# Performance work log

Hardware: AMD Instinct MI355X
Metric: run time of the kernel (lower is better)

Reference implementation:

```python
import jax, jax.numpy as jnp
import numpy as np

N_NODES = 100000
K_NBRS = 16
N_EDGES = N_NODES * K_NBRS


def setup_inputs() -> dict:
    key = jax.random.key(0)
    ks = jax.random.split(key, 20)
    x = jax.random.normal(ks[0], (N_NODES, 3), dtype=jnp.float32)
    # knn-like edge list: every node is the target of exactly K_NBRS edges
    dst = jnp.repeat(jnp.arange(N_NODES, dtype=jnp.int64), K_NBRS)
    src = jax.random.randint(ks[1], (N_EDGES,), 0, N_NODES, dtype=jnp.int64)
    edge_index = jnp.stack([src, dst], axis=0)  # [2, E], row0=source(j), row1=target(i)

    def lin_init(k, fan_in, fan_out):
        s = 1.0 / np.sqrt(fan_in)
        return jax.random.uniform(k, (fan_in, fan_out), jnp.float32, -s, s)

    inp = {"x": x, "edge_index": edge_index}
    inp["W1"], inp["b1"] = lin_init(ks[2], 6, 64), jnp.zeros((64,), jnp.float32)
    for i, kk in zip(range(2, 6), ks[3:7]):
        inp[f"W{i}"] = lin_init(kk, 128, 64)
        inp[f"b{i}"] = jnp.zeros((64,), jnp.float32)
    inp["Wa"], inp["ba"] = lin_init(ks[8], 128, 128), jnp.zeros((128,), jnp.float32)
    inp["Wb"], inp["bb"] = lin_init(ks[9], 128, 3), jnp.zeros((3,), jnp.float32)
    return inp


def edge_conv(x, src, dst, W, b):
    # PyG EdgeConv: message = nn(cat([x_i, x_j - x_i])), max-aggregate at target i
    xi = x[dst]                      # [E, C] center (target) features
    xj = x[src]                      # [E, C] neighbor (source) features
    msg = jnp.concatenate([xi, xj - xi], axis=-1)  # [E, 2C]
    msg = jax.nn.relu(msg @ W + b)                 # [E, 64] per-edge MLP
    return jax.ops.segment_max(msg, dst, num_segments=N_NODES)  # [N, 64]


def reference(x, edge_index, W1, b1, W2, b2, W3, b3, W4, b4, W5, b5, Wa, ba, Wb, bb):
    src, dst = edge_index[0], edge_index[1]
    h = edge_conv(x, src, dst, W1, b1)
    h = edge_conv(h, src, dst, W2, b2)
    h = edge_conv(h, src, dst, W3, b3)
    h = edge_conv(h, src, dst, W4, b4)
    h = edge_conv(h, src, dst, W5, b5)           # [N, 64]
    g = jnp.max(h, axis=0, keepdims=True)        # [1, 64] global max
    feat = jnp.concatenate([h, jnp.broadcast_to(g, h.shape)], axis=1)  # [N, 128]
    out = jax.nn.relu(feat @ Wa + ba) @ Wb + bb  # [N, 3]
    return x + out
```

## Files before the change

### kernel.cpp

```cpp
#include <hip/hip_runtime.h>
#include <math.h>

#define N_NODES 100000
#define K_NBRS 16
#define N_EDGES (N_NODES * K_NBRS)
#define TPB 256
#define NBLK 2048
#define NTILES (N_NODES / 16)

typedef __attribute__((ext_vector_type(8))) short short8;
typedef __attribute__((ext_vector_type(4))) float float4_;
typedef __attribute__((ext_vector_type(4))) int int4_;
typedef __attribute__((ext_vector_type(4))) unsigned short ushort4_;

__device__ __forceinline__ unsigned short f2bf(float f) {
  unsigned int u = __float_as_uint(f);
  u += 0x7fffu + ((u >> 16) & 1u);
  return (unsigned short)(u >> 16);
}
__device__ __forceinline__ float bf2f(unsigned short b) {
  return __uint_as_float(((unsigned int)b) << 16);
}

__global__ void k_pre(const int* __restrict__ ei, int* __restrict__ srcout,
                      const float* __restrict__ x, const float* __restrict__ W1,
                      const float* __restrict__ b1,
                      unsigned short* __restrict__ A, unsigned short* __restrict__ B) {
  const bool is64 = (ei[1] == 0) && (ei[3] == 0) && (ei[5] == 0) && (ei[7] == 0);
  const int tid = blockIdx.x * blockDim.x + threadIdx.x;
  const int stride = gridDim.x * blockDim.x;
  for (int e = tid; e < N_EDGES; e += stride)
    srcout[e] = is64 ? ei[2 * e] : ei[e];

  const int lane = threadIdx.x & 63;
  const int nwaves = stride >> 6;
  const int wid0 = tid >> 6;
  float w[6];
#pragma unroll
  for (int k = 0; k < 6; ++k) w[k] = W1[k * 64 + lane];
  const float bias = b1[lane];
  for (int i0 = wid0; i0 < N_NODES; i0 += nwaves) {
    const int i = __builtin_amdgcn_readfirstlane(i0);
    const float x0 = x[3 * i], x1 = x[3 * i + 1], x2 = x[3 * i + 2];
    const float b = fmaf(x0, w[3], fmaf(x1, w[4], x2 * w[5]));
    const float a = bias + fmaf(x0, w[0] - w[3],
                          fmaf(x1, w[1] - w[4], x2 * (w[2] - w[5])));
    A[(size_t)i * 64 + lane] = f2bf(a);
    B[(size_t)i * 64 + lane] = f2bf(b);
  }
}

__global__ __launch_bounds__(TPB, 4)
void k_fused(const int* __restrict__ src,
             const unsigned short* __restrict__ Ain,
             const unsigned short* __restrict__ Bin,
             const float* __restrict__ W, const float* __restrict__ bn,
             unsigned short* __restrict__ Aout, unsigned short* __restrict__ Bout) {
  __shared__ __align__(16) unsigned short lwhi[128 * 72];
  __shared__ __align__(16) unsigned short lwlo[128 * 72];
  __shared__ __align__(16) unsigned short lh[16 * 72];
  for (int idx = threadIdx.x; idx < 8192; idx += TPB) {
    const int k = idx >> 7, j = idx & 127;
    const float v = (j < 64) ? (W[k * 64 + j] - W[(64 + k) * 64 + j])
                             : W[(64 + k) * 64 + (j - 64)];
    const unsigned short hi = f2bf(v);
    lwhi[j * 72 + k] = hi;
    lwlo[j * 72 + k] = f2bf(v - bf2f(hi));
  }
  const int lane = threadIdx.x & 63;
  const int wav = threadIdx.x >> 6;
  const int q = lane >> 4;
  const int l15 = lane & 15;
  const int c4 = l15 * 4;
  float bv0 = 0.f, bv1 = 0.f;
  if (wav < 2) {
    bv0 = bn[(2 * wav) * 16 + l15];
    bv1 = bn[(2 * wav + 1) * 16 + l15];
  }
  __syncthreads();
  for (int t = blockIdx.x; t < NTILES; t += gridDim.x) {
    const int i0 = t * 16 + wav * 4;
    int4_ idx[4];
#pragma unroll
    for (int n = 0; n < 4; ++n)
      idx[n] = *(const int4_*)(src + (size_t)(i0 + n) * 16 + q * 4);
    ushort4_ gv[4][4];
#pragma unroll
    for (int n = 0; n < 4; ++n)
#pragma unroll
      for (int e = 0; e < 4; ++e)
        gv[n][e] = *(const ushort4_*)(Bin + (size_t)idx[n][e] * 64 + c4);
    const ushort4_ av = *(const ushort4_*)(Ain + (size_t)(i0 + q) * 64 + c4);
    float4_ m[4];
#pragma unroll
    for (int n = 0; n < 4; ++n) {
#pragma unroll
      for (int tt = 0; tt < 4; ++tt) {
        const float v0 = bf2f(gv[n][0][tt]), v1 = bf2f(gv[n][1][tt]);
        const float v2 = bf2f(gv[n][2][tt]), v3 = bf2f(gv[n][3][tt]);
        m[n][tt] = fmaxf(fmaxf(v0, v1), fmaxf(v2, v3));
      }
#pragma unroll
      for (int tt = 0; tt < 4; ++tt) {
        float v = m[n][tt];
        v = fmaxf(v, __shfl_xor(v, 16));
        v = fmaxf(v, __shfl_xor(v, 32));
        m[n][tt] = v;
      }
    }
    ushort4_ hb;
#pragma unroll
    for (int tt = 0; tt < 4; ++tt) {
      float v = m[0][tt];
      v = (q == 1) ? m[1][tt] : v;
      v = (q == 2) ? m[2][tt] : v;
      v = (q == 3) ? m[3][tt] : v;
      hb[tt] = f2bf(fmaxf(bf2f(av[tt]) + v, 0.f));
    }
    *(ushort4_*)&lh[(wav * 4 + q) * 72 + c4] = hb;
    __syncthreads();
    const short8 a0 = *(const short8*)&lh[l15 * 72 + q * 8];
    const short8 a1 = *(const short8*)&lh[l15 * 72 + 32 + q * 8];
    float4_ acc0 = (float4_)(0.f), acc1 = (float4_)(0.f);
    {
      const int ct0 = wav * 2, ct1 = wav * 2 + 1;
      const int r0 = (ct0 * 16 + l15) * 72 + q * 8;
      const int r1 = (ct1 * 16 + l15) * 72 + q * 8;
      acc0 = __builtin_amdgcn_mfma_f32_16x16x32_bf16(a0, *(const short8*)&lwhi[r0], acc0, 0, 0, 0);
      acc0 = __builtin_amdgcn_mfma_f32_16x16x32_bf16(a0, *(const short8*)&lwlo[r0], acc0, 0, 0, 0);
      acc0 = __builtin_amdgcn_mfma_f32_16x16x32_bf16(a1, *(const short8*)&lwhi[r0 + 32], acc0, 0, 0, 0);
      acc0 = __builtin_amdgcn_mfma_f32_16x16x32_bf16(a1, *(const short8*)&lwlo[r0 + 32], acc0, 0, 0, 0);
      acc1 = __builtin_amdgcn_mfma_f32_16x16x32_bf16(a0, *(const short8*)&lwhi[r1], acc1, 0, 0, 0);
      acc1 = __builtin_amdgcn_mfma_f32_16x16x32_bf16(a0, *(const short8*)&lwlo[r1], acc1, 0, 0, 0);
      acc1 = __builtin_amdgcn_mfma_f32_16x16x32_bf16(a1, *(const short8*)&lwhi[r1 + 32], acc1, 0, 0, 0);
      acc1 = __builtin_amdgcn_mfma_f32_16x16x32_bf16(a1, *(const short8*)&lwlo[r1 + 32], acc1, 0, 0, 0);
    }
#pragma unroll
    for (int r = 0; r < 4; ++r) {
      const int node = t * 16 + q * 4 + r;
      const int ct0 = wav * 2, ct1 = wav * 2 + 1;
      if (wav < 2) {
        Aout[(size_t)node * 64 + ct0 * 16 + l15] = f2bf(acc0[r] + bv0);
        Aout[(size_t)node * 64 + ct1 * 16 + l15] = f2bf(acc1[r] + bv1);
      } else {
        Bout[(size_t)node * 64 + (ct0 - 4) * 16 + l15] = f2bf(acc0[r]);
        Bout[(size_t)node * 64 + (ct1 - 4) * 16 + l15] = f2bf(acc1[r]);
      }
    }
    __syncthreads();
  }
}

__global__ void k_aggr_last(const int* __restrict__ src,
                            const unsigned short* __restrict__ Ain,
                            const unsigned short* __restrict__ Bin,
                            unsigned short* __restrict__ hout, float* __restrict__ P) {
  const int lane = threadIdx.x & 63;
  const int q = lane >> 4;
  const int c4 = (lane & 15) * 4;
  const int nw = (gridDim.x * blockDim.x) >> 6;
  const int w0 = (blockIdx.x * blockDim.x + threadIdx.x) >> 6;
  float4_ gmax = (float4_)(0.f);
  for (int p = w0; p * 4 < N_NODES; p += nw) {
    const int i0 = __builtin_amdgcn_readfirstlane(p * 4);
    int4_ idx[4];
#pragma unroll
    for (int n = 0; n < 4; ++n)
      idx[n] = *(const int4_*)(src + (size_t)(i0 + n) * 16 + q * 4);
    ushort4_ gv[4][4];
#pragma unroll
    for (int n = 0; n < 4; ++n)
#pragma unroll
      for (int e = 0; e < 4; ++e)
        gv[n][e] = *(const ushort4_*)(Bin + (size_t)idx[n][e] * 64 + c4);
    const ushort4_ av = *(const ushort4_*)(Ain + (size_t)(i0 + q) * 64 + c4);
    float4_ m[4];
#pragma unroll
    for (int n = 0; n < 4; ++n) {
#pragma unroll
      for (int tt = 0; tt < 4; ++tt) {
        const float v0 = bf2f(gv[n][0][tt]), v1 = bf2f(gv[n][1][tt]);
        const float v2 = bf2f(gv[n][2][tt]), v3 = bf2f(gv[n][3][tt]);
        m[n][tt] = fmaxf(fmaxf(v0, v1), fmaxf(v2, v3));
      }
#pragma unroll
      for (int tt = 0; tt < 4; ++tt) {
        float v = m[n][tt];
        v = fmaxf(v, __shfl_xor(v, 16));
        v = fmaxf(v, __shfl_xor(v, 32));
        m[n][tt] = v;
      }
    }
    ushort4_ hb;
#pragma unroll
    for (int tt = 0; tt < 4; ++tt) {
      float v = m[0][tt];
      v = (q == 1) ? m[1][tt] : v;
      v = (q == 2) ? m[2][tt] : v;
      v = (q == 3) ? m[3][tt] : v;
      const float h = fmaxf(bf2f(av[tt]) + v, 0.f);
      hb[tt] = f2bf(h);
      gmax[tt] = fmaxf(gmax[tt], h);
    }
    *(ushort4_*)(hout + (size_t)(i0 + q) * 64 + c4) = hb;
  }
  __shared__ float red[TPB][4];
#pragma unroll
  for (int tt = 0; tt < 4; ++tt) red[threadIdx.x][tt] = gmax[tt];
  __syncthreads();
  if (threadIdx.x < 64) {
    const int c = threadIdx.x, j = c >> 2, tt = c & 3;
    float mm = 0.f;
#pragma unroll
    for (int w = 0; w < 4; ++w)
#pragma unroll
      for (int qq = 0; qq < 4; ++qq)
        mm = fmaxf(mm, red[w * 64 + qq * 16 + j][tt]);
    P[(size_t)blockIdx.x * 64 + c] = mm;
  }
}

__global__ void k_gred(const float* __restrict__ P, float* __restrict__ g) {
  __shared__ float red[16][64];
  const int lane = threadIdx.x & 63;
  const int w = threadIdx.x >> 6;
  float m = 0.f;
  for (int r = w; r < NBLK; r += 16)
    m = fmaxf(m, P[(size_t)r * 64 + lane]);
  red[w][lane] = m;
  __syncthreads();
  if (threadIdx.x < 64) {
    float mm = 0.f;
#pragma unroll
    for (int k = 0; k < 16; ++k) mm = fmaxf(mm, red[k][lane]);
    g[lane] = mm;
  }
}

__global__ __launch_bounds__(TPB, 2)
void k_final(const unsigned short* __restrict__ h, const float* __restrict__ g,
             const float* __restrict__ Wa, const float* __restrict__ ba,
             const float* __restrict__ Wb, const float* __restrict__ bb,
             const float* __restrict__ x, float* __restrict__ out) {
  __shared__ __align__(16) unsigned short lwhi[128 * 72];
  __shared__ __align__(16) unsigned short lwlo[128 * 72];
  __shared__ float sgt[128];
  for (int idx = threadIdx.x; idx < 8192; idx += TPB) {
    const int k = idx >> 7, j = idx & 127;
    const float v = Wa[k * 128 + j];
    const unsigned short hi = f2bf(v);
    lwhi[j * 72 + k] = hi;
    lwlo[j * 72 + k] = f2bf(v - bf2f(hi));
  }
  if (threadIdx.x < 128) {
    const int c = threadIdx.x;
    float s = ba[c];
    for (int k = 0; k < 64; ++k) s = fmaf(g[k], Wa[(64 + k) * 128 + c], s);
    sgt[c] = s;
  }
  __syncthreads();
  const int lane = threadIdx.x & 63;
  const int wav = threadIdx.x >> 6;
  const int l15 = lane & 15, lg = lane >> 4;
  short8 bhi[8][2], blo[8][2];
#pragma unroll
  for (int ct = 0; ct < 8; ++ct)
#pragma unroll
    for (int kk = 0; kk < 2; ++kk) {
      const int off = (ct * 16 + l15) * 72 + kk * 32 + lg * 8;
      bhi[ct][kk] = *(const short8*)&lwhi[off];
      blo[ct][kk] = *(const short8*)&lwlo[off];
    }
  float gtv[8];
#pragma unroll
  for (int ct = 0; ct < 8; ++ct) gtv[ct] = sgt[ct * 16 + l15];
  float wbv[8][3];
#pragma unroll
  for (int ct = 0; ct < 8; ++ct)
#pragma unroll
    for (int jj = 0; jj < 3; ++jj)
      wbv[ct][jj] = Wb[(ct * 16 + l15) * 3 + jj];
  const float bbl = (l15 == 0) ? bb[0] : (l15 == 1 ? bb[1] : bb[2]);
  const int NT = (N_NODES + 63) / 64;
  for (int t = blockIdx.x; t < NT; t += gridDim.x) {
    const int nb = t * 64 + wav * 16;
    const int row = min(nb + l15, N_NODES - 1);
    const unsigned short* hr = h + (size_t)row * 64;
    float4_ acc[8];
#pragma unroll
    for (int ct = 0; ct < 8; ++ct) acc[ct] = (float4_)(0.f);
#pragma unroll
    for (int kk = 0; kk < 2; ++kk) {
      const short8 ahi = *(const short8*)(hr + kk * 32 + lg * 8);
#pragma unroll
      for (int ct = 0; ct < 8; ++ct) {
        acc[ct] = __builtin_amdgcn_mfma_f32_16x16x32_bf16(ahi, bhi[ct][kk], acc[ct], 0, 0, 0);
        acc[ct] = __builtin_amdgcn_mfma_f32_16x16x32_bf16(ahi, blo[ct][kk], acc[ct], 0, 0, 0);
      }
    }
#pragma unroll
    for (int r = 0; r < 4; ++r) {
      float t0 = 0.f, t1 = 0.f, t2 = 0.f;
#pragma unroll
      for (int ct = 0; ct < 8; ++ct) {
        const float hd = fmaxf(acc[ct][r] + gtv[ct], 0.f);
        t0 = fmaf(hd, wbv[ct][0], t0);
        t1 = fmaf(hd, wbv[ct][1], t1);
        t2 = fmaf(hd, wbv[ct][2], t2);
      }
#pragma unroll
      for (int off = 1; off < 16; off <<= 1) {
        t0 += __shfl_xor(t0, off);
        t1 += __shfl_xor(t1, off);
        t2 += __shfl_xor(t2, off);
      }
      const int node = nb + lg * 4 + r;
      if (node < N_NODES && l15 < 3) {
        const float tj = (l15 == 0) ? t0 : (l15 == 1 ? t1 : t2);
        out[(size_t)node * 3 + l15] = x[(size_t)node * 3 + l15] + tj + bbl;
      }
    }
  }
}

extern "C" void kernel_launch(void* const* d_in, const int* in_sizes, int n_in,
                              void* d_out, int out_size, void* d_ws, size_t ws_size,
                              hipStream_t stream) {
  const float* x  = (const float*)d_in[0];
  const int*   ei = (const int*)d_in[1];
  const float* W1 = (const float*)d_in[2];
  const float* b1 = (const float*)d_in[3];
  const float* W2 = (const float*)d_in[4];
  const float* b2 = (const float*)d_in[5];
  const float* W3 = (const float*)d_in[6];
  const float* b3 = (const float*)d_in[7];
  const float* W4 = (const float*)d_in[8];
  const float* b4 = (const float*)d_in[9];
  const float* W5 = (const float*)d_in[10];
  const float* b5 = (const float*)d_in[11];
  const float* Wa = (const float*)d_in[12];
  const float* ba = (const float*)d_in[13];
  const float* Wb = (const float*)d_in[14];
  const float* bb = (const float*)d_in[15];
  float* out = (float*)d_out;

  float* ws = (float*)d_ws;
  int* srcbuf = (int*)ws;
  unsigned short* A0 = (unsigned short*)(ws + 1600000);
  unsigned short* B0 = A0 + 6400000;
  unsigned short* A1 = B0 + 6400000;
  unsigned short* B1 = A1 + 6400000;
  unsigned short* H  = B1 + 6400000;
  float* P = (float*)(H + 6400000);
  float* g = P + (size_t)NBLK * 64;

  k_pre<<<NBLK, TPB, 0, stream>>>(ei, srcbuf, x, W1, b1, A0, B0);
  k_fused<<<NBLK, TPB, 0, stream>>>(srcbuf, A0, B0, W2, b2, A1, B1);
  k_fused<<<NBLK, TPB, 0, stream>>>(srcbuf, A1, B1, W3, b3, A0, B0);
  k_fused<<<NBLK, TPB, 0, stream>>>(srcbuf, A0, B0, W4, b4, A1, B1);
  k_fused<<<NBLK, TPB, 0, stream>>>(srcbuf, A1, B1, W5, b5, A0, B0);
  k_aggr_last<<<NBLK, TPB, 0, stream>>>(srcbuf, A0, B0, H, P);
  k_gred<<<1, 1024, 0, stream>>>(P, g);
  k_final<<<512, TPB, 0, stream>>>(H, g, Wa, ba, Wb, bb, x, out);
}
```

Baseline: 374.6 us.

## Software-pipeline fused EdgeConv tiles with double-buffered LDS and register-resident weights

Restructures the fused EdgeConv loop so the neighbor gather for the next tile is issued before the MFMA and store of the current tile. The activation staging buffer is double-buffered in LDS, which removes one barrier per tile, and uses an XOR-swizzled layout to avoid bank conflicts. Weight fragments are loaded into registers once per block rather than re-read from LDS every tile. Grid size is cut to 1250 blocks (5 tiles each), which trades fewer blocks and higher register pressure for overlap of gather latency with compute.

```diff
diff --git a/kernel.cpp b/kernel.cpp
--- a/kernel.cpp
+++ b/kernel.cpp
@@ -7,6 +7,7 @@
 #define TPB 256
 #define NBLK 2048
 #define NTILES (N_NODES / 16)
+#define NBLK_F 1250
 
 typedef __attribute__((ext_vector_type(8))) short short8;
 typedef __attribute__((ext_vector_type(4))) float float4_;
@@ -58,7 +59,7 @@
              unsigned short* __restrict__ Aout, unsigned short* __restrict__ Bout) {
   __shared__ __align__(16) unsigned short lwhi[128 * 72];
   __shared__ __align__(16) unsigned short lwlo[128 * 72];
-  __shared__ __align__(16) unsigned short lh[16 * 72];
+  __shared__ __align__(16) unsigned short lh[2][16 * 64];
   for (int idx = threadIdx.x; idx < 8192; idx += TPB) {
     const int k = idx >> 7, j = idx & 127;
     const float v = (j < 64) ? (W[k * 64 + j] - W[(64 + k) * 64 + j])
@@ -78,19 +79,33 @@
     bv1 = bn[(2 * wav + 1) * 16 + l15];
   }
   __syncthreads();
-  for (int t = blockIdx.x; t < NTILES; t += gridDim.x) {
+  short8 whi[2][2], wlo[2][2];
+#pragma unroll
+  for (int tt = 0; tt < 2; ++tt)
+#pragma unroll
+    for (int kk = 0; kk < 2; ++kk) {
+      const int off = ((wav * 2 + tt) * 16 + l15) * 72 + kk * 32 + q * 8;
+      whi[tt][kk] = *(const short8*)&lwhi[off];
+      wlo[tt][kk] = *(const short8*)&lwlo[off];
+    }
+  const int wrow = wav * 4 + q;
+  const int wr_off = wrow * 64 + ((((l15 >> 1) ^ (wrow & 7))) << 3) + ((l15 & 1) << 2);
+  const int rd0 = l15 * 64 + ((q ^ (l15 & 7)) << 3);
+  const int rd1 = l15 * 64 + (((q + 4) ^ (l15 & 7)) << 3);
+
+  auto gather_issue = [&](int t, int4_ idx[4], ushort4_ gv[4][4], ushort4_& av) {
     const int i0 = t * 16 + wav * 4;
-    int4_ idx[4];
 #pragma unroll
     for (int n = 0; n < 4; ++n)
       idx[n] = *(const int4_*)(src + (size_t)(i0 + n) * 16 + q * 4);
-    ushort4_ gv[4][4];
 #pragma unroll
     for (int n = 0; n < 4; ++n)
 #pragma unroll
       for (int e = 0; e < 4; ++e)
         gv[n][e] = *(const ushort4_*)(Bin + (size_t)idx[n][e] * 64 + c4);
-    const ushort4_ av = *(const ushort4_*)(Ain + (size_t)(i0 + q) * 64 + c4);
+    av = *(const ushort4_*)(Ain + (size_t)(i0 + q) * 64 + c4);
+  };
+  auto reduce_write = [&](const ushort4_ gv[4][4], ushort4_ av, int buf) {
     float4_ m[4];
 #pragma unroll
     for (int n = 0; n < 4; ++n) {
@@ -117,28 +132,24 @@
       v = (q == 3) ? m[3][tt] : v;
       hb[tt] = f2bf(fmaxf(bf2f(av[tt]) + v, 0.f));
     }
-    *(ushort4_*)&lh[(wav * 4 + q) * 72 + c4] = hb;
-    __syncthreads();
-    const short8 a0 = *(const short8*)&lh[l15 * 72 + q * 8];
-    const short8 a1 = *(const short8*)&lh[l15 * 72 + 32 + q * 8];
+    *(ushort4_*)&lh[buf][wr_off] = hb;
+  };
+  auto mma_store = [&](int t, int buf) {
+    const short8 a0 = *(const short8*)&lh[buf][rd0];
+    const short8 a1 = *(const short8*)&lh[buf][rd1];
     float4_ acc0 = (float4_)(0.f), acc1 = (float4_)(0.f);
-    {
-      const int ct0 = wav * 2, ct1 = wav * 2 + 1;
-      const int r0 = (ct0 * 16 + l15) * 72 + q * 8;
-      const int r1 = (ct1 * 16 + l15) * 72 + q * 8;
-      acc0 = __builtin_amdgcn_mfma_f32_16x16x32_bf16(a0, *(const short8*)&lwhi[r0], acc0, 0, 0, 0);
-      acc0 = __builtin_amdgcn_mfma_f32_16x16x32_bf16(a0, *(const short8*)&lwlo[r0], acc0, 0, 0, 0);
-      acc0 = __builtin_amdgcn_mfma_f32_16x16x32_bf16(a1, *(const short8*)&lwhi[r0 + 32], acc0, 0, 0, 0);
-      acc0 = __builtin_amdgcn_mfma_f32_16x16x32_bf16(a1, *(const short8*)&lwlo[r0 + 32], acc0, 0, 0, 0);
-      acc1 = __builtin_amdgcn_mfma_f32_16x16x32_bf16(a0, *(const short8*)&lwhi[r1], acc1, 0, 0, 0);
-      acc1 = __builtin_amdgcn_mfma_f32_16x16x32_bf16(a0, *(const short8*)&lwlo[r1], acc1, 0, 0, 0);
-      acc1 = __builtin_amdgcn_mfma_f32_16x16x32_bf16(a1, *(const short8*)&lwhi[r1 + 32], acc1, 0, 0, 0);
-      acc1 = __builtin_amdgcn_mfma_f32_16x16x32_bf16(a1, *(const short8*)&lwlo[r1 + 32], acc1, 0, 0, 0);
-    }
+    acc0 = __builtin_amdgcn_mfma_f32_16x16x32_bf16(a0, whi[0][0], acc0, 0, 0, 0);
+    acc0 = __builtin_amdgcn_mfma_f32_16x16x32_bf16(a0, wlo[0][0], acc0, 0, 0, 0);
+    acc0 = __builtin_amdgcn_mfma_f32_16x16x32_bf16(a1, whi[0][1], acc0, 0, 0, 0);
+    acc0 = __builtin_amdgcn_mfma_f32_16x16x32_bf16(a1, wlo[0][1], acc0, 0, 0, 0);
+    acc1 = __builtin_amdgcn_mfma_f32_16x16x32_bf16(a0, whi[1][0], acc1, 0, 0, 0);
+    acc1 = __builtin_amdgcn_mfma_f32_16x16x32_bf16(a0, wlo[1][0], acc1, 0, 0, 0);
+    acc1 = __builtin_amdgcn_mfma_f32_16x16x32_bf16(a1, whi[1][1], acc1, 0, 0, 0);
+    acc1 = __builtin_amdgcn_mfma_f32_16x16x32_bf16(a1, wlo[1][1], acc1, 0, 0, 0);
+    const int ct0 = wav * 2, ct1 = wav * 2 + 1;
 #pragma unroll
     for (int r = 0; r < 4; ++r) {
       const int node = t * 16 + q * 4 + r;
-      const int ct0 = wav * 2, ct1 = wav * 2 + 1;
       if (wav < 2) {
         Aout[(size_t)node * 64 + ct0 * 16 + l15] = f2bf(acc0[r] + bv0);
         Aout[(size_t)node * 64 + ct1 * 16 + l15] = f2bf(acc1[r] + bv1);
@@ -147,7 +158,26 @@
         Bout[(size_t)node * 64 + (ct1 - 4) * 16 + l15] = f2bf(acc1[r]);
       }
     }
+  };
+
+  int4_ idx[4];
+  ushort4_ gv[4][4];
+  ushort4_ av;
+  int t = blockIdx.x;
+  gather_issue(t, idx, gv, av);
+  reduce_write(gv, av, 0);
+  __syncthreads();
+  int cur = 0;
+  while (true) {
+    const int tn = t + NBLK_F;
+    const bool hn = tn < NTILES;
+    if (hn) gather_issue(tn, idx, gv, av);
+    mma_store(t, cur);
+    if (!hn) break;
+    reduce_write(gv, av, cur ^ 1);
     __syncthreads();
+    cur ^= 1;
+    t = tn;
   }
 }
 
@@ -355,10 +385,10 @@
   float* g = P + (size_t)NBLK * 64;
 
   k_pre<<<NBLK, TPB, 0, stream>>>(ei, srcbuf, x, W1, b1, A0, B0);
-  k_fused<<<NBLK, TPB, 0, stream>>>(srcbuf, A0, B0, W2, b2, A1, B1);
-  k_fused<<<NBLK, TPB, 0, stream>>>(srcbuf, A1, B1, W3, b3, A0, B0);
-  k_fused<<<NBLK, TPB, 0, stream>>>(srcbuf, A0, B0, W4, b4, A1, B1);
-  k_fused<<<NBLK, TPB, 0, stream>>>(srcbuf, A1, B1, W5, b5, A0, B0);
+  k_fused<<<NBLK_F, TPB, 0, stream>>>(srcbuf, A0, B0, W2, b2, A1, B1);
+  k_fused<<<NBLK_F, TPB, 0, stream>>>(srcbuf, A1, B1, W3, b3, A0, B0);
+  k_fused<<<NBLK_F, TPB, 0, stream>>>(srcbuf, A0, B0, W4, b4, A1, B1);
+  k_fused<<<NBLK_F, TPB, 0, stream>>>(srcbuf, A1, B1, W5, b5, A0, B0);
   k_aggr_last<<<NBLK, TPB, 0, stream>>>(srcbuf, A0, B0, H, P);
   k_gred<<<1, 1024, 0, stream>>>(P, g);
   k_final<<<512, TPB, 0, stream>>>(H, g, Wa, ba, Wb, bb, x, out);
```

After: 376.4 us. About the same (+0.5%).
